# Performance work log

Hardware: AMD Instinct MI355X
Metric: run time of the kernel (lower is better)

## Reference

```python
import jax, jax.numpy as jnp
import numpy as np

SEQ, BATCH, IN, HID, OUT = 512, 4096, 9, 64, 10


def setup_inputs() -> dict:
    key = jax.random.key(0)
    ks = jax.random.split(key, 11)
    s = 1.0 / np.sqrt(HID)
    u = lambda k, shp: jax.random.uniform(k, shp, jnp.float32, -s, s)
    return {
        "x": jax.random.normal(ks[0], (SEQ, BATCH, IN), jnp.float32),
        "W_ih0": u(ks[1], (HID, IN)),
        "W_hh0": u(ks[2], (HID, HID)),
        "b_ih0": u(ks[3], (HID,)),
        "b_hh0": u(ks[4], (HID,)),
        "W_ih1": u(ks[5], (HID, HID)),
        "W_hh1": u(ks[6], (HID, HID)),
        "b_ih1": u(ks[7], (HID,)),
        "b_hh1": u(ks[8], (HID,)),
        "W_fc": u(ks[9], (OUT, HID)),
        "b_fc": u(ks[10], (OUT,)),
    }


def _rnn_layer(x, W_ih, W_hh, b_ih, b_hh):
    # x: (seq, batch, d_in) -> (seq, batch, hid); h_t = tanh(x_t W_ih^T + b_ih + h_{t-1} W_hh^T + b_hh)
    xw = jnp.einsum('sbi,hi->sbh', x, W_ih) + (b_ih + b_hh)  # precompute input proj
    h0 = jnp.zeros((x.shape[1], W_hh.shape[0]), x.dtype)

    def step(h, xw_t):
        h = jnp.tanh(xw_t + h @ W_hh.T)
        return h, h

    _, out = jax.lax.scan(step, h0, xw)
    return out


def reference(x, W_ih0, W_hh0, b_ih0, b_hh0, W_ih1, W_hh1, b_ih1, b_hh1, W_fc, b_fc):
    h1 = _rnn_layer(x, W_ih0, W_hh0, b_ih0, b_hh0)   # (seq, batch, hid)
    h2 = _rnn_layer(h1, W_ih1, W_hh1, b_ih1, b_hh1)  # (seq, batch, hid)
    # Faithful to original quirk: rnn_out[:, -1, :] on a (seq, batch, hid) tensor
    # selects the last BATCH element for every timestep -> (seq, hid)
    feat = h2[:, -1, :]
    return feat @ W_fc.T + b_fc  # (seq, out)
```

## Files before the change

kernel.cpp:

```cpp
#include <hip/hip_runtime.h>

#define SEQn   512
#define BATCHn 4096
#define INn    9
#define HIDn   64
#define OUTn   10
#define ROW1   72
#define U2P    72

typedef __attribute__((ext_vector_type(4))) float    f32x4;
typedef __attribute__((ext_vector_type(4))) _Float16 f16x4;
typedef _Float16 half2_t __attribute__((ext_vector_type(2)));
typedef unsigned short u16;
typedef unsigned int   u32;

#define MFMA16(A,B,C) __builtin_amdgcn_mfma_f32_16x16x16f16((A),(B),(C),0,0,0)

#if __has_builtin(__builtin_amdgcn_fdot2)
#define DOT2(a,b,c) __builtin_amdgcn_fdot2((a),(b),(c),false)
#else
__device__ __forceinline__ float DOT2(half2_t a, half2_t b, float c){
    return __builtin_fmaf((float)a.x,(float)b.x, __builtin_fmaf((float)a.y,(float)b.y,c));
}
#endif
#define H2(u) __builtin_bit_cast(half2_t, (u))

__device__ __forceinline__ float tanh_pre(float x){
    float e = __builtin_amdgcn_exp2f(x);
    float r = __builtin_amdgcn_rcpf(e + 1.0f);
    return __builtin_fmaf(-2.0f, r, 1.0f);
}
__device__ __forceinline__ u16 f2h(float v){ return __builtin_bit_cast(u16, (_Float16)v); }
__device__ __forceinline__ f16x4 cvt4(f32x4 a){
    f16x4 r = {(_Float16)a.x, (_Float16)a.y, (_Float16)a.z, (_Float16)a.w};
    return r;
}

__device__ __forceinline__ void load_w16s(const float* __restrict__ W, int row, float s, half2_t* wr){
#pragma unroll
    for (int c = 0; c < 16; ++c){
        f32x4 v = *(const f32x4*)&W[row*HIDn + c*4];
        wr[2*c]   = half2_t{(_Float16)(v.x*s), (_Float16)(v.y*s)};
        wr[2*c+1] = half2_t{(_Float16)(v.z*s), (_Float16)(v.w*s)};
    }
}

__device__ __forceinline__ float dot64r(const uint4* v, const half2_t* wr, float acc){
    float a0 = acc, a1 = 0.f, a2 = 0.f, a3 = 0.f;
#pragma unroll
    for (int jb = 0; jb < 8; ++jb){
        a0 = DOT2(H2(v[jb].x), wr[jb*4+0], a0);
        a1 = DOT2(H2(v[jb].y), wr[jb*4+1], a1);
        a2 = DOT2(H2(v[jb].z), wr[jb*4+2], a2);
        a3 = DOT2(H2(v[jb].w), wr[jb*4+3], a3);
    }
    return (a0 + a1) + (a2 + a3);
}

extern "C" __global__ __launch_bounds__(256, 1)
void rnn_lastrow(const float* __restrict__ x,
                 const float* __restrict__ Wih0, const float* __restrict__ Whh0,
                 const float* __restrict__ bih0, const float* __restrict__ bhh0,
                 const float* __restrict__ Wih1, const float* __restrict__ Whh1,
                 const float* __restrict__ bih1, const float* __restrict__ bhh1,
                 const float* __restrict__ Wfc,  const float* __restrict__ bfc,
                 float* __restrict__ out)
{
    __shared__ __align__(16) u16   xl16[SEQn*16];
    __shared__ __align__(16) float u2r[64*U2P];
    __shared__ __align__(16) u16   ring1[16*ROW1];
    __shared__ __align__(16) u16   ring2[16*ROW1];
    __shared__ u32 wm[2];

    const int tid  = threadIdx.x;
    const int w    = tid >> 6;
    const int lane = tid & 63;
    const int g    = lane >> 4;
    const int n    = lane & 15;
    volatile u32* vwm = wm;
    const float K = 2.8853900817779268f;

    for (int idx = tid; idx < SEQn*16; idx += 256){
        int t = idx >> 4, j = idx & 15;
        float v = (j < INn) ? x[((long)t*BATCHn + (BATCHn-1))*INn + j] : 0.f;
        xl16[idx] = f2h(v);
    }
    for (int idx = tid; idx < 16*ROW1; idx += 256){ ring1[idx] = 0; ring2[idx] = 0; }
    if (tid == 0){ wm[0] = 0u; wm[1] = 0u; }
    __syncthreads();
    if (w >= 2) return;

    if (w == 0){
        half2_t wr0[32], wx[5];
        load_w16s(Whh0, lane, K, wr0);
        {
            const float* wxr = Wih0 + lane*INn;
#pragma unroll
            for (int q = 0; q < 4; ++q)
                wx[q] = half2_t{(_Float16)(wxr[2*q]*K), (_Float16)(wxr[2*q+1]*K)};
            wx[4] = half2_t{(_Float16)(wxr[8]*K), (_Float16)0.f};
        }
        const float b1 = (bih0[lane] + bhh0[lane]) * K;

        f16x4 wi1[4][4]; f32x4 b2f[4];
#pragma unroll
        for (int r = 0; r < 4; ++r){
            f32x4 bi1 = *(const f32x4*)&bih1[16*r + 4*g];
            f32x4 bh1 = *(const f32x4*)&bhh1[16*r + 4*g];
            b2f[r] = (bi1 + bh1) * K;
#pragma unroll
            for (int c = 0; c < 4; ++c){
                f32x4 a1 = *(const f32x4*)&Wih1[(16*r + n)*HIDn + 16*c + 4*g];
                wi1[r][c] = cvt4(a1 * K);
            }
        }

        auto u2batch = [&](int p0){
            f16x4 B[4];
#pragma unroll
            for (int c = 0; c < 4; ++c)
                B[c] = *(const f16x4*)&ring1[n*ROW1 + 16*c + 4*g];
            f32x4 D[4];
#pragma unroll
            for (int r = 0; r < 4; ++r) D[r] = b2f[r];
#pragma unroll
            for (int c = 0; c < 4; ++c)
#pragma unroll
                for (int r = 0; r < 4; ++r)
                    D[r] = MFMA16(wi1[r][c], B[c], D[r]);
            int t = (p0 - 16 + n) & 63;
#pragma unroll
            for (int r = 0; r < 4; ++r)
                *(f32x4*)&u2r[t*U2P + 16*r + 4*g] = D[r];
        };

        for (int p = 0; p < SEQn; ++p){
            if ((p & 15) == 0 && p){
                int guard = 1 << 20;
                while ((vwm[1] + 64u <= (u32)p) && --guard) __builtin_amdgcn_s_sleep(2);
                asm volatile("" ::: "memory");
                u2batch(p);
                asm volatile("s_waitcnt lgkmcnt(0)" ::: "memory");
                vwm[0] = (u32)p;
            }
            const u32* xr = (const u32*)(xl16 + p*16);
            uint4 xa = *(const uint4*)xr;
            u32  xb  = xr[4];
            uint4 CUR[8];
            const uint4* hrow = (const uint4*)(ring1 + ((p-1) & 15)*ROW1);
#pragma unroll
            for (int j = 0; j < 8; ++j) CUR[j] = hrow[j];
            float u1 = b1;
            u1 = DOT2(H2(xa.x), wx[0], u1);
            u1 = DOT2(H2(xa.y), wx[1], u1);
            u1 = DOT2(H2(xa.z), wx[2], u1);
            u1 = DOT2(H2(xa.w), wx[3], u1);
            u1 = DOT2(H2(xb),   wx[4], u1);
            float y = dot64r(CUR, wr0, u1);
            ring1[(p & 15)*ROW1 + lane] = f2h(tanh_pre(y));
        }
        {
            int guard = 1 << 20;
            while ((vwm[1] + 64u <= (u32)SEQn) && --guard) __builtin_amdgcn_s_sleep(2);
            asm volatile("" ::: "memory");
            u2batch(SEQn);
            asm volatile("s_waitcnt lgkmcnt(0)" ::: "memory");
            vwm[0] = (u32)SEQn;
        }
    } else {
        half2_t wr2[32];
        load_w16s(Whh1, lane, K, wr2);
        f16x4 wfcA[4]; f32x4 bfcf;
        {
            int mrow = (n < OUTn) ? n : (OUTn - 1);
#pragma unroll
            for (int c = 0; c < 4; ++c)
                wfcA[c] = cvt4(*(const f32x4*)&Wfc[mrow*HIDn + 16*c + 4*g]);
            int o0 = 4*g;
            bfcf.x = (o0+0 < OUTn) ? bfc[o0+0] : 0.f;
            bfcf.y = (o0+1 < OUTn) ? bfc[o0+1] : 0.f;
            bfcf.z = (o0+2 < OUTn) ? bfc[o0+2] : 0.f;
            bfcf.w = (o0+3 < OUTn) ? bfc[o0+3] : 0.f;
        }

        auto fcbatch = [&](int c0){
            f16x4 B[4];
#pragma unroll
            for (int c = 0; c < 4; ++c)
                B[c] = *(const f16x4*)&ring2[n*ROW1 + 16*c + 4*g];
            f32x4 D = bfcf;
#pragma unroll
            for (int c = 0; c < 4; ++c)
                D = MFMA16(wfcA[c], B[c], D);
            int t = c0 - 16 + n;
            float* o = out + t*OUTn + 4*g;
            if (g < 2){ o[0] = D.x; o[1] = D.y; o[2] = D.z; o[3] = D.w; }
            else if (g == 2){ o[0] = D.x; o[1] = D.y; }
        };

        for (int c = 0; c < SEQn; ++c){
            if ((c & 15) == 0){
                vwm[1] = (u32)c;
                if (c) fcbatch(c);
                int guard = 1 << 20;
                while ((vwm[0] < (u32)(c + 16)) && --guard) __builtin_amdgcn_s_sleep(1);
                asm volatile("" ::: "memory");
            }
            float u2v = u2r[(c & 63)*U2P + lane];
            uint4 CUR[8];
            const uint4* hrow = (const uint4*)(ring2 + ((c-1) & 15)*ROW1);
#pragma unroll
            for (int j = 0; j < 8; ++j) CUR[j] = hrow[j];
            float y = dot64r(CUR, wr2, u2v);
            ring2[(c & 15)*ROW1 + lane] = f2h(tanh_pre(y));
        }
        fcbatch(SEQn);
    }
}

extern "C" void kernel_launch(void* const* d_in, const int* in_sizes, int n_in,
                              void* d_out, int out_size, void* d_ws, size_t ws_size,
                              hipStream_t stream){
    rnn_lastrow<<<dim3(1), dim3(256), 0, stream>>>(
        (const float*)d_in[0],
        (const float*)d_in[1], (const float*)d_in[2],
        (const float*)d_in[3], (const float*)d_in[4],
        (const float*)d_in[5], (const float*)d_in[6],
        (const float*)d_in[7], (const float*)d_in[8],
        (const float*)d_in[9], (const float*)d_in[10],
        (float*)d_out);
}
```

Before: 241.1 us.

## Split RNN pipeline into four wavefronts with dedicated input-projection and FC waves

Moves the layer-2 input projection (MFMA batch) off the layer-1 recurrence wave and the FC output batch off the layer-2 recurrence wave. Each now runs in its own wavefront, so all four waves work and the two serial recurrence loops no longer stall on batched MFMA work. The hidden-state rings grow from 16 to 64 rows to decouple producers from consumers, with new watermark flags for flow control. The 64-wide dot product also uses eight independent accumulators instead of four to shorten the dependency chain. The cost is more spin-wait synchronisation between waves and a more complex set of ring-overwrite conditions.

```diff
diff --git a/kernel.cpp b/kernel.cpp
--- a/kernel.cpp
+++ b/kernel.cpp
@@ -45,16 +45,20 @@
     }
 }
 
-__device__ __forceinline__ float dot64r(const uint4* v, const half2_t* wr, float acc){
-    float a0 = acc, a1 = 0.f, a2 = 0.f, a3 = 0.f;
-#pragma unroll
-    for (int jb = 0; jb < 8; ++jb){
-        a0 = DOT2(H2(v[jb].x), wr[jb*4+0], a0);
-        a1 = DOT2(H2(v[jb].y), wr[jb*4+1], a1);
-        a2 = DOT2(H2(v[jb].z), wr[jb*4+2], a2);
-        a3 = DOT2(H2(v[jb].w), wr[jb*4+3], a3);
-    }
-    return (a0 + a1) + (a2 + a3);
+__device__ __forceinline__ float dot64r8(const uint4* v, const half2_t* wr, float acc){
+    float s0=acc, s1=0.f, s2=0.f, s3=0.f, s4=0.f, s5=0.f, s6=0.f, s7=0.f;
+#pragma unroll
+    for (int q = 0; q < 4; ++q){
+        s0 = DOT2(H2(v[2*q].x),   wr[8*q+0], s0);
+        s1 = DOT2(H2(v[2*q].y),   wr[8*q+1], s1);
+        s2 = DOT2(H2(v[2*q].z),   wr[8*q+2], s2);
+        s3 = DOT2(H2(v[2*q].w),   wr[8*q+3], s3);
+        s4 = DOT2(H2(v[2*q+1].x), wr[8*q+4], s4);
+        s5 = DOT2(H2(v[2*q+1].y), wr[8*q+5], s5);
+        s6 = DOT2(H2(v[2*q+1].z), wr[8*q+6], s6);
+        s7 = DOT2(H2(v[2*q+1].w), wr[8*q+7], s7);
+    }
+    return ((s0+s1)+(s2+s3)) + ((s4+s5)+(s6+s7));
 }
 
 extern "C" __global__ __launch_bounds__(256, 1)
@@ -68,9 +72,9 @@
 {
     __shared__ __align__(16) u16   xl16[SEQn*16];
     __shared__ __align__(16) float u2r[64*U2P];
-    __shared__ __align__(16) u16   ring1[16*ROW1];
-    __shared__ __align__(16) u16   ring2[16*ROW1];
-    __shared__ u32 wm[2];
+    __shared__ __align__(16) u16   ring1[64*ROW1];
+    __shared__ __align__(16) u16   ring2[64*ROW1];
+    __shared__ u32 wm[4];
 
     const int tid  = threadIdx.x;
     const int w    = tid >> 6;
@@ -85,10 +89,9 @@
         float v = (j < INn) ? x[((long)t*BATCHn + (BATCHn-1))*INn + j] : 0.f;
         xl16[idx] = f2h(v);
     }
-    for (int idx = tid; idx < 16*ROW1; idx += 256){ ring1[idx] = 0; ring2[idx] = 0; }
-    if (tid == 0){ wm[0] = 0u; wm[1] = 0u; }
+    for (int idx = tid; idx < 64*ROW1; idx += 256){ ring1[idx] = 0; ring2[idx] = 0; }
+    if (tid < 4) wm[tid] = 0u;
     __syncthreads();
-    if (w >= 2) return;
 
     if (w == 0){
         half2_t wr0[32], wx[5];
@@ -102,52 +105,19 @@
         }
         const float b1 = (bih0[lane] + bhh0[lane]) * K;
 
-        f16x4 wi1[4][4]; f32x4 b2f[4];
-#pragma unroll
-        for (int r = 0; r < 4; ++r){
-            f32x4 bi1 = *(const f32x4*)&bih1[16*r + 4*g];
-            f32x4 bh1 = *(const f32x4*)&bhh1[16*r + 4*g];
-            b2f[r] = (bi1 + bh1) * K;
-#pragma unroll
-            for (int c = 0; c < 4; ++c){
-                f32x4 a1 = *(const f32x4*)&Wih1[(16*r + n)*HIDn + 16*c + 4*g];
-                wi1[r][c] = cvt4(a1 * K);
-            }
-        }
-
-        auto u2batch = [&](int p0){
-            f16x4 B[4];
-#pragma unroll
-            for (int c = 0; c < 4; ++c)
-                B[c] = *(const f16x4*)&ring1[n*ROW1 + 16*c + 4*g];
-            f32x4 D[4];
-#pragma unroll
-            for (int r = 0; r < 4; ++r) D[r] = b2f[r];
-#pragma unroll
-            for (int c = 0; c < 4; ++c)
-#pragma unroll
-                for (int r = 0; r < 4; ++r)
-                    D[r] = MFMA16(wi1[r][c], B[c], D[r]);
-            int t = (p0 - 16 + n) & 63;
-#pragma unroll
-            for (int r = 0; r < 4; ++r)
-                *(f32x4*)&u2r[t*U2P + 16*r + 4*g] = D[r];
-        };
-
         for (int p = 0; p < SEQn; ++p){
             if ((p & 15) == 0 && p){
-                int guard = 1 << 20;
-                while ((vwm[1] + 64u <= (u32)p) && --guard) __builtin_amdgcn_s_sleep(2);
-                asm volatile("" ::: "memory");
-                u2batch(p);
                 asm volatile("s_waitcnt lgkmcnt(0)" ::: "memory");
                 vwm[0] = (u32)p;
+                int guard = 1 << 20;
+                while ((vwm[1] + 48u < (u32)p) && --guard) __builtin_amdgcn_s_sleep(2);
+                asm volatile("" ::: "memory");
             }
             const u32* xr = (const u32*)(xl16 + p*16);
             uint4 xa = *(const uint4*)xr;
             u32  xb  = xr[4];
             uint4 CUR[8];
-            const uint4* hrow = (const uint4*)(ring1 + ((p-1) & 15)*ROW1);
+            const uint4* hrow = (const uint4*)(ring1 + ((p-1) & 63)*ROW1);
 #pragma unroll
             for (int j = 0; j < 8; ++j) CUR[j] = hrow[j];
             float u1 = b1;
@@ -156,20 +126,74 @@
             u1 = DOT2(H2(xa.z), wx[2], u1);
             u1 = DOT2(H2(xa.w), wx[3], u1);
             u1 = DOT2(H2(xb),   wx[4], u1);
-            float y = dot64r(CUR, wr0, u1);
-            ring1[(p & 15)*ROW1 + lane] = f2h(tanh_pre(y));
-        }
-        {
+            float y = dot64r8(CUR, wr0, u1);
+            ring1[(p & 63)*ROW1 + lane] = f2h(tanh_pre(y));
+        }
+        asm volatile("s_waitcnt lgkmcnt(0)" ::: "memory");
+        vwm[0] = (u32)SEQn;
+    } else if (w == 2){
+        f16x4 wi1[4][4]; f32x4 b2f[4];
+#pragma unroll
+        for (int r = 0; r < 4; ++r){
+            f32x4 bi1 = *(const f32x4*)&bih1[16*r + 4*g];
+            f32x4 bh1 = *(const f32x4*)&bhh1[16*r + 4*g];
+            b2f[r] = (bi1 + bh1) * K;
+#pragma unroll
+            for (int c = 0; c < 4; ++c){
+                f32x4 a1 = *(const f32x4*)&Wih1[(16*r + n)*HIDn + 16*c + 4*g];
+                wi1[r][c] = cvt4(a1 * K);
+            }
+        }
+        for (int b = 1; b <= 32; ++b){
+            int t0 = 16*b;
             int guard = 1 << 20;
-            while ((vwm[1] + 64u <= (u32)SEQn) && --guard) __builtin_amdgcn_s_sleep(2);
+            while ((vwm[0] < (u32)t0) && --guard) __builtin_amdgcn_s_sleep(2);
+            guard = 1 << 20;
+            while ((vwm[2] + 64u < (u32)t0) && --guard) __builtin_amdgcn_s_sleep(2);
             asm volatile("" ::: "memory");
-            u2batch(SEQn);
+            f16x4 B[4];
+#pragma unroll
+            for (int c = 0; c < 4; ++c)
+                B[c] = *(const f16x4*)&ring1[((t0-16+n) & 63)*ROW1 + 16*c + 4*g];
+            f32x4 D[4];
+#pragma unroll
+            for (int r = 0; r < 4; ++r) D[r] = b2f[r];
+#pragma unroll
+            for (int c = 0; c < 4; ++c)
+#pragma unroll
+                for (int r = 0; r < 4; ++r)
+                    D[r] = MFMA16(wi1[r][c], B[c], D[r]);
+            int t = (t0 - 16 + n) & 63;
+#pragma unroll
+            for (int r = 0; r < 4; ++r)
+                *(f32x4*)&u2r[t*U2P + 16*r + 4*g] = D[r];
             asm volatile("s_waitcnt lgkmcnt(0)" ::: "memory");
-            vwm[0] = (u32)SEQn;
-        }
-    } else {
+            vwm[1] = (u32)t0;
+        }
+    } else if (w == 1){
         half2_t wr2[32];
         load_w16s(Whh1, lane, K, wr2);
+        for (int c = 0; c < SEQn; ++c){
+            if ((c & 15) == 0){
+                asm volatile("s_waitcnt lgkmcnt(0)" ::: "memory");
+                vwm[2] = (u32)c;
+                int guard = 1 << 20;
+                while ((vwm[1] < (u32)(c + 16)) && --guard) __builtin_amdgcn_s_sleep(2);
+                guard = 1 << 20;
+                while ((vwm[3] + 48u < (u32)c) && --guard) __builtin_amdgcn_s_sleep(2);
+                asm volatile("" ::: "memory");
+            }
+            float u2v = u2r[(c & 63)*U2P + lane];
+            uint4 CUR[8];
+            const uint4* hrow = (const uint4*)(ring2 + ((c-1) & 63)*ROW1);
+#pragma unroll
+            for (int j = 0; j < 8; ++j) CUR[j] = hrow[j];
+            float y = dot64r8(CUR, wr2, u2v);
+            ring2[(c & 63)*ROW1 + lane] = f2h(tanh_pre(y));
+        }
+        asm volatile("s_waitcnt lgkmcnt(0)" ::: "memory");
+        vwm[2] = (u32)SEQn;
+    } else {
         f16x4 wfcA[4]; f32x4 bfcf;
         {
             int mrow = (n < OUTn) ? n : (OUTn - 1);
@@ -182,39 +206,26 @@
             bfcf.z = (o0+2 < OUTn) ? bfc[o0+2] : 0.f;
             bfcf.w = (o0+3 < OUTn) ? bfc[o0+3] : 0.f;
         }
-
-        auto fcbatch = [&](int c0){
+        for (int b = 1; b <= 32; ++b){
+            int f0 = 16*b;
+            int guard = 1 << 20;
+            while ((vwm[2] < (u32)f0) && --guard) __builtin_amdgcn_s_sleep(2);
+            asm volatile("" ::: "memory");
             f16x4 B[4];
 #pragma unroll
             for (int c = 0; c < 4; ++c)
-                B[c] = *(const f16x4*)&ring2[n*ROW1 + 16*c + 4*g];
+                B[c] = *(const f16x4*)&ring2[((f0-16+n) & 63)*ROW1 + 16*c + 4*g];
             f32x4 D = bfcf;
 #pragma unroll
             for (int c = 0; c < 4; ++c)
                 D = MFMA16(wfcA[c], B[c], D);
-            int t = c0 - 16 + n;
+            int t = f0 - 16 + n;
             float* o = out + t*OUTn + 4*g;
             if (g < 2){ o[0] = D.x; o[1] = D.y; o[2] = D.z; o[3] = D.w; }
             else if (g == 2){ o[0] = D.x; o[1] = D.y; }
-        };
-
-        for (int c = 0; c < SEQn; ++c){
-            if ((c & 15) == 0){
-                vwm[1] = (u32)c;
-                if (c) fcbatch(c);
-                int guard = 1 << 20;
-                while ((vwm[0] < (u32)(c + 16)) && --guard) __builtin_amdgcn_s_sleep(1);
-                asm volatile("" ::: "memory");
-            }
-            float u2v = u2r[(c & 63)*U2P + lane];
-            uint4 CUR[8];
-            const uint4* hrow = (const uint4*)(ring2 + ((c-1) & 15)*ROW1);
-#pragma unroll
-            for (int j = 0; j < 8; ++j) CUR[j] = hrow[j];
-            float y = dot64r(CUR, wr2, u2v);
-            ring2[(c & 15)*ROW1 + lane] = f2h(tanh_pre(y));
-        }
-        fcbatch(SEQn);
+            asm volatile("s_waitcnt lgkmcnt(0)" ::: "memory");
+            vwm[3] = (u32)f0;
+        }
     }
 }
 
```

Result: no change. 238.1 us (-1.2%).
